# Optimization experiments

Measured on AMD Instinct MI355X. Metric: run time of the kernel, lower is better.

## Reference

```python
import jax, jax.numpy as jnp
import numpy as np

# CUBA-LIF constants (from LavaNetwork.__init__ with beta=0.95)
THRESHOLD = 1.0
CURRENT_DECAY = 1.0   # current[t] = (1-1.0)*current[t-1] + input[t] == input[t]
VOLTAGE_DECAY = 1.0 - 0.95  # = 0.05, so v[t] = 0.95*v[t-1] + cur[t]

N_INPUT, N_HIDDEN, N_OUTPUT = 512, 2048, 4 * 64
B, T = 32, 1024


def setup_inputs() -> dict:
    key = jax.random.key(0)
    kx, k1, k2, k3, k4 = jax.random.split(key, 5)
    x = (jax.random.uniform(kx, (B, N_INPUT, T)) < 0.1).astype(jnp.float32)
    # learned params (Linear with bias); small scale so spiking is reasonable
    w1 = jax.random.normal(k1, (N_HIDDEN, N_INPUT), dtype=jnp.float32) * (1.0 / np.sqrt(N_INPUT))
    b1 = jax.random.normal(k2, (N_HIDDEN,), dtype=jnp.float32) * 0.01
    w2 = jax.random.normal(k3, (N_OUTPUT, N_HIDDEN), dtype=jnp.float32) * (1.0 / np.sqrt(N_HIDDEN))
    b2 = jax.random.normal(k4, (N_OUTPUT,), dtype=jnp.float32) * 0.01
    return {"x": x, "w1": w1, "b1": b1, "w2": w2, "b2": b2}


def _cuba_lif(cur):
    """CUBA neuron with current_decay=1 (current==synaptic input),
    leaky-integrate voltage, fire at threshold, reset voltage to 0.
    cur: (B, N, T) -> spikes (B, N, T)."""
    beta_v = 1.0 - VOLTAGE_DECAY  # 0.95

    def step(v, c_t):
        v = v * beta_v + c_t
        s = (v >= THRESHOLD).astype(v.dtype)
        v = v * (1.0 - s)  # reset-to-zero on spike (Loihi behavior)
        return v, s

    cur_t = jnp.moveaxis(cur, -1, 0)  # (T, B, N)
    v0 = jnp.zeros(cur.shape[:-1], cur.dtype)
    _, spk = jax.lax.scan(step, v0, cur_t)
    return jnp.moveaxis(spk, 0, -1)  # (B, N, T)


def reference(x, w1, b1, w2, b2):
    # layer 1: synapse (einsum 'bit,oi->bot' + bias) -> CUBA neuron
    cur1 = jnp.einsum('bit,oi->bot', x, w1) + b1[None, :, None]
    spk1 = _cuba_lif(cur1)
    # layer 2
    cur2 = jnp.einsum('bit,oi->bot', spk1, w2) + b2[None, :, None]
    spk2 = _cuba_lif(cur2)
    return (spk1, spk2)
```

## Files before the change

kernel.cpp:

```cpp
#include <hip/hip_runtime.h>


typedef int i32x4 __attribute__((ext_vector_type(4)));
typedef _Float16 f16x8 __attribute__((ext_vector_type(8)));
typedef _Float16 f16x4 __attribute__((ext_vector_type(4)));
typedef float f32x4 __attribute__((ext_vector_type(4)));

#define GLDS(g, l) __builtin_amdgcn_global_load_lds( \
    (const __attribute__((address_space(1))) void*)(g), \
    (__attribute__((address_space(3))) void*)(l), 16, 0, 0)

#define INV231 4.656612873077392578125e-10


__global__ __launch_bounds__(256) void prep_w8(const float* __restrict__ A,
                                               signed char* __restrict__ wp,
                                               int M, int K)
{
    long gt = (long)blockIdx.x * 256 + threadIdx.x;
    int kq4 = K >> 2;
    int m = (int)(gt / kq4), kq = (int)(gt % kq4);
    int k0 = kq * 4;
    int kt = k0 >> 6, kin = k0 & 63;
    int cw = ((kin >> 4) ^ (m >> 1)) & 3;
    float4 w = *(const float4*)&A[(long)m * K + k0];
    float wv[4] = {w.x, w.y, w.z, w.w};
    int pack[4] = {0, 0, 0, 0};
#pragma unroll
    for (int e = 0; e < 4; e++) {
        long k64 = (long)rint((double)wv[e] * 2147483648.0);
#pragma unroll
        for (int j = 0; j < 3; j++) {
            long r = ((k64 + 128) & 255) - 128;
            pack[j] |= ((int)r & 255) << (e * 8);
            k64 = (k64 - r) >> 8;
        }
        pack[3] |= ((int)k64 & 255) << (e * 8);
    }
#pragma unroll
    for (int p = 0; p < 4; p++)
        *(int*)&wp[(((long)kt * 4 + p) * M + m) * 64 + cw * 16 + (kin & 15)] = pack[p];
}

__global__ __launch_bounds__(256) void prep_x8(const float* __restrict__ x,
                                               unsigned char* __restrict__ xt)
{
    __shared__ float xs[64][68];
    const int b = blockIdx.z, i0 = blockIdx.y * 64, t0 = blockIdx.x * 64;
    const float* xb = x + ((long)b * 512 + i0) * 1024 + t0;
#pragma unroll
    for (int p = 0; p < 4; p++) {
        int f = threadIdx.x + p * 256;
        int i = f >> 4, t4 = (f & 15) * 4;
        *(float4*)&xs[i][t4] = *(const float4*)&xb[(long)i * 1024 + t4];
    }
    __syncthreads();
    int tt = threadIdx.x >> 2, c = threadIdx.x & 3;
    unsigned char bytes[16];
#pragma unroll
    for (int j = 0; j < 16; j++)
        bytes[j] = (unsigned char)xs[c * 16 + j][tt];
    *(uint4*)&xt[(((long)b * 8 + (i0 >> 6)) * 1024 + t0 + tt) * 64 + c * 16] =
        *(uint4*)bytes;
}

__global__ __launch_bounds__(320, 1) void gemm_lif1(
    const signed char* __restrict__ wp,
    const unsigned char* __restrict__ act,
    const float* __restrict__ bias,
    unsigned char* __restrict__ spk8,
    float* __restrict__ spk1)
{
    __shared__ signed char Ws[8][4][64][64];
    __shared__ float cs[2][64][64];

    const int m0 = blockIdx.x * 64, b = blockIdx.y;
    const int tid = threadIdx.x, lane = tid & 63, wave = tid >> 6;
    const int lm = lane & 15, lq = lane >> 4;
    const int fro = ((lq ^ (lm >> 1)) & 3) * 16;
    const unsigned char* ab = act + (long)b * 8 * 1024 * 64;

    unsigned char* sp8 = spk8 + (((long)b * 32 + (m0 >> 6)) * 1024) * 64 + lane;
    float* sp1 = spk1 + ((long)b * 2048 + m0) * 1024;

    i32x4 areg[4][4];
    double bv = 0.0;

    if (wave < 4) {
        const int gl_row = lane >> 2, gl_col = (lane & 3) * 16;
#pragma unroll
        for (int j = 0; j < 8; ++j) {
            const int r = wave + 4 * j;
            const int kt = r >> 2, pl = r & 3;
            const signed char* g = wp + ((long)r * 2048 + m0 + gl_row) * 64 + gl_col;
#pragma unroll
            for (int q = 0; q < 4; ++q)
                GLDS(g + q * 16 * 64, &Ws[kt][pl][q * 16][0]);
        }
        bv = (double)bias[m0 + wave * 16 + lm];
#pragma unroll
        for (int f = 0; f < 4; f++)
            areg[0][f] = *(const i32x4*)
                &ab[((long)(f * 16 + lm)) * 64 + lq * 16];
#pragma unroll
        for (int f = 0; f < 4; f++)
            areg[1][f] = *(const i32x4*)
                &ab[((long)1 * 1024 + f * 16 + lm) * 64 + lq * 16];
    }
    __syncthreads();

    double u = 0.0;
    bool sprev = false;

    for (int p = 0; p < 17; ++p) {
        if (wave < 4 && p < 16) {
            i32x4 acc[4][4];
#pragma unroll
            for (int pp = 0; pp < 4; pp++)
#pragma unroll
                for (int f = 0; f < 4; f++) acc[pp][f] = (i32x4)0;

            i32x4 wreg[4];
            wreg[0] = *(const i32x4*)&Ws[0][0][wave * 16 + lm][fro];
            wreg[1] = *(const i32x4*)&Ws[0][1][wave * 16 + lm][fro];

#pragma unroll
            for (int kk = 0; kk < 8; ++kk) {
                {
                    int vn = p * 8 + kk + 2;
                    if (vn > 127) vn = 127;
                    const int pn = vn >> 3, kn = vn & 7;
                    const long tt = (long)pn * 64 + lm;
#pragma unroll
                    for (int f = 0; f < 4; f++)
                        areg[(kk + 2) & 3][f] = *(const i32x4*)
                            &ab[((long)kn * 1024 + tt + f * 16) * 64 + lq * 16];
                }
                __builtin_amdgcn_s_setprio(1);
#pragma unroll
                for (int pl = 0; pl < 4; pl++) {
                    const int q = kk * 4 + pl;
                    const int qn = q + 2;
                    if (qn < 32)
                        wreg[qn & 3] = *(const i32x4*)
                            &Ws[qn >> 2][qn & 3][wave * 16 + lm][fro];
#pragma unroll
                    for (int f = 0; f < 4; f++)
                        acc[pl][f] = __builtin_amdgcn_mfma_i32_16x16x64_i8(
                            areg[kk & 3][f], wreg[q & 3], acc[pl][f], 0, 0, 0);
                }
                __builtin_amdgcn_s_setprio(0);
            }
#pragma unroll
            for (int tf = 0; tf < 4; tf++)
#pragma unroll
                for (int r = 0; r < 4; r++) {
                    long T = acc[3][tf][r];
                    T = T * 256 + acc[2][tf][r];
                    T = T * 256 + acc[1][tf][r];
                    T = T * 256 + acc[0][tf][r];
                    cs[p & 1][tf * 16 + lq * 4 + r][wave * 16 + lm] =
                        (float)((double)T * INV231 + bv);
                }
        }
        if (wave == 4 && p >= 1) {
            const int pq = p - 1, buf = pq & 1;
            float cvA[32], cvB[32];
#pragma unroll
            for (int j = 0; j < 32; ++j) cvA[j] = cs[buf][j][lane];
#pragma unroll
            for (int j = 0; j < 32; ++j) cvB[j] = cs[buf][32 + j][lane];
            unsigned mwordA = 0, mwordB = 0;
#pragma unroll
            for (int j = 0; j < 32; ++j) {
                double c = (double)cvA[j];
                double a = 0.95 * u + c;
                u = sprev ? c : a;
                bool s = (u >= 1.0);
                mwordA |= (s ? 1u : 0u) << j;
                sprev = s;
                sp8[(long)(pq * 64 + j) * 64] = s ? 1 : 0;
            }
#pragma unroll
            for (int j = 0; j < 32; ++j) {
                double c = (double)cvB[j];
                double a = 0.95 * u + c;
                u = sprev ? c : a;
                bool s = (u >= 1.0);
                mwordB |= (s ? 1u : 0u) << j;
                sprev = s;
                sp8[(long)(pq * 64 + 32 + j) * 64] = s ? 1 : 0;
            }
            float* sp1t = sp1 + pq * 64 + lane;
#pragma unroll 4
            for (int mm = 0; mm < 64; ++mm) {
                unsigned wa = (unsigned)__shfl((int)mwordA, mm);
                unsigned wb = (unsigned)__shfl((int)mwordB, mm);
                unsigned sel = (lane < 32) ? wa : wb;
                sp1t[(long)mm * 1024] =
                    ((sel >> (lane & 31)) & 1u) ? 1.f : 0.f;
            }
        }
        asm volatile("s_waitcnt lgkmcnt(0)" ::: "memory");
        __builtin_amdgcn_s_barrier();
        __builtin_amdgcn_sched_barrier(0);
    }
}

template <bool TRANS, int NITER, int CHUNK>
__global__ __launch_bounds__(256, 2) void gemm_i8(
    const signed char* __restrict__ wp,
    const unsigned char* __restrict__ act,
    const float* __restrict__ bias,
    float* __restrict__ C,
    int M)
{
    constexpr int NCHUNK = NITER / CHUNK;
    __shared__ signed char Ws[CHUNK][4][32][64];

    const int b = blockIdx.y;
    const int m0 = blockIdx.z * 32, t0 = blockIdx.x * 256;
    const int tid = threadIdx.x, lane = tid & 63, wave = tid >> 6;
    const int wt = t0 + wave * 64;
    const int lm = lane & 15, lq = lane >> 4;
    const int fro = ((lq ^ (lm >> 1)) & 3) * 16;
    const int gl_row = lane >> 2, gl_col = (lane & 3) * 16;

    const unsigned char* ab = act + (long)b * NITER * 1024 * 64;

    auto stage = [&](int cc) {
#pragma unroll
        for (int j = 0; j < CHUNK; ++j) {
            const int r = wave + 4 * j;
            const int kt = r >> 2, p = r & 3;
            const long kg = ((long)(cc * CHUNK + kt) * 4 + p);
            const signed char* g = wp + (kg * M + m0 + gl_row) * 64 + gl_col;
            GLDS(g, &Ws[kt][p][0][0]);
            GLDS(g + 16 * 64, &Ws[kt][p][16][0]);
        }
    };

    i32x4 acc[4][8];
#pragma unroll
    for (int p = 0; p < 4; p++)
#pragma unroll
        for (int q = 0; q < 8; q++) acc[p][q] = (i32x4)0;

    stage(0);
    i32x4 areg[2][4];
#pragma unroll
    for (int f = 0; f < 4; f++)
        areg[0][f] = *(const i32x4*)&ab[((long)(wt + f * 16 + lm)) * 64 + lq * 16];
    __syncthreads();

    for (int c = 0; c < NCHUNK; ++c) {
#pragma unroll
        for (int kk = 0; kk < CHUNK; ++kk) {
            {
                const int itv = c * CHUNK + kk;
                const long nx = (itv + 1 < NITER) ? itv + 1 : itv;
#pragma unroll
                for (int f = 0; f < 4; f++)
                    areg[(kk + 1) & 1][f] = *(const i32x4*)
                        &ab[(nx * 1024 + wt + f * 16 + lm) * 64 + lq * 16];
            }
#pragma unroll
            for (int p = 0; p < 4; p++) {
                i32x4 w0 = *(const i32x4*)&Ws[kk][p][lm][fro];
                i32x4 w1 = *(const i32x4*)&Ws[kk][p][16 + lm][fro];
                if (TRANS) {
#pragma unroll
                    for (int f = 0; f < 4; f++) {
                        acc[p][f * 2 + 0] = __builtin_amdgcn_mfma_i32_16x16x64_i8(
                            areg[kk & 1][f], w0, acc[p][f * 2 + 0], 0, 0, 0);
                        acc[p][f * 2 + 1] = __builtin_amdgcn_mfma_i32_16x16x64_i8(
                            areg[kk & 1][f], w1, acc[p][f * 2 + 1], 0, 0, 0);
                    }
                } else {
#pragma unroll
                    for (int f = 0; f < 4; f++) {
                        acc[p][0 + f] = __builtin_amdgcn_mfma_i32_16x16x64_i8(
                            w0, areg[kk & 1][f], acc[p][0 + f], 0, 0, 0);
                        acc[p][4 + f] = __builtin_amdgcn_mfma_i32_16x16x64_i8(
                            w1, areg[kk & 1][f], acc[p][4 + f], 0, 0, 0);
                    }
                }
            }
        }
        if (c + 1 < NCHUNK) {
            __syncthreads();
            stage(c + 1);
            __syncthreads();
        }
    }

    if (TRANS) {
        double bv[2];
        bv[0] = (double)bias[m0 + lm];
        bv[1] = (double)bias[m0 + 16 + lm];
        float* Cb = C + (long)b * 1024 * M;
#pragma unroll
        for (int tf = 0; tf < 4; tf++)
#pragma unroll
            for (int r = 0; r < 4; r++) {
                const int trow = wt + tf * 16 + lq * 4 + r;
#pragma unroll
                for (int mf = 0; mf < 2; mf++) {
                    long T = acc[3][tf * 2 + mf][r];
                    T = T * 256 + acc[2][tf * 2 + mf][r];
                    T = T * 256 + acc[1][tf * 2 + mf][r];
                    T = T * 256 + acc[0][tf * 2 + mf][r];
                    Cb[(long)trow * M + m0 + mf * 16 + lm] =
                        (float)((double)T * INV231 + bv[mf]);
                }
            }
    } else {
        float* Cb = C + (long)b * M * 1024;
#pragma unroll
        for (int mf = 0; mf < 2; mf++)
#pragma unroll
            for (int r = 0; r < 4; r++) {
                const int mrow = m0 + mf * 16 + lq * 4 + r;
                const double bv = (double)bias[mrow];
#pragma unroll
                for (int tf = 0; tf < 4; tf++) {
                    long T = acc[3][mf * 4 + tf][r];
                    T = T * 256 + acc[2][mf * 4 + tf][r];
                    T = T * 256 + acc[1][mf * 4 + tf][r];
                    T = T * 256 + acc[0][mf * 4 + tf][r];
                    Cb[(long)mrow * 1024 + wt + tf * 16 + lm] =
                        (float)((double)T * INV231 + bv);
                }
            }
    }
}

template <int RPB>
__global__ __launch_bounds__(256) void lif_lds(float* __restrict__ cur)
{
    __shared__ float cs[RPB][36];
    const long rowbase = (long)blockIdx.x * RPB;
    float* base = cur + rowbase * 1024;
    const int tid = threadIdx.x;
    double v = 0.0;
    const int NV = RPB * 32 / 4;
    for (int tc = 0; tc < 1024; tc += 32) {
        for (int f = tid; f < NV; f += 256) {
            int row = f >> 3, t4 = (f & 7) * 4;
            *(float4*)&cs[row][t4] = *(const float4*)&base[(long)row * 1024 + tc + t4];
        }
        __syncthreads();
        if (tid < RPB) {
            float cv[32];
#pragma unroll
            for (int j = 0; j < 32; j++) cv[j] = cs[tid][j];
#pragma unroll
            for (int j = 0; j < 32; j++) {
                v = 0.95 * v + (double)cv[j];
                bool s = v >= 1.0;
                cs[tid][j] = s ? 1.f : 0.f;
                if (s) v = 0.0;
            }
        }
        __syncthreads();
        for (int f = tid; f < NV; f += 256) {
            int row = f >> 3, t4 = (f & 7) * 4;
            *(float4*)&base[(long)row * 1024 + tc + t4] = *(float4*)&cs[row][t4];
        }
        __syncthreads();
    }
}


__device__ inline void split3(float w, _Float16& q0, _Float16& q1, _Float16& q2) {
    float p0 = rintf(w * 4096.f) * 2.44140625e-4f;
    float r1 = w - p0;
    float p1s = rintf(r1 * 8388608.f) * 2.44140625e-4f;
    float r2 = r1 - p1s * 4.8828125e-4f;
    float p2s = rintf(r2 * 1.7179869184e10f) * 1.220703125e-4f;
    q0 = (_Float16)p0; q1 = (_Float16)p1s; q2 = (_Float16)p2s;
}

__global__ __launch_bounds__(256) void gemm_f16x3_kernel(
    const float* __restrict__ A, const float* __restrict__ Bmat,
    const float* __restrict__ bias, float* __restrict__ C,
    int M, int N, int K, long sB, long sC)
{
    __shared__ _Float16 As[3][128][40];
    __shared__ _Float16 Bsh[128][40];
    const int batch = blockIdx.z;
    const float* Bp = Bmat + (long)batch * sB;
    float* Cp = C + (long)batch * sC;
    const int m0 = blockIdx.y * 128, n0 = blockIdx.x * 128;
    const int tid = threadIdx.x, lane = tid & 63, wave = tid >> 6;
    const int wrow = (wave >> 1) * 64, wcol = (wave & 1) * 64;
    const int lm = lane & 15, lq = lane >> 4;
    const int a_mo = tid >> 3, a_kc = (tid & 7) * 4;
    const int b_kq = tid >> 5, b_nq = tid & 31;

    f32x4 acc[3][4][4];
#pragma unroll
    for (int p = 0; p < 3; p++)
#pragma unroll
        for (int i = 0; i < 4; i++)
#pragma unroll
            for (int j = 0; j < 4; j++) acc[p][i][j] = (f32x4)0.f;

    for (int k0 = 0; k0 < K; k0 += 32) {
#pragma unroll
        for (int i = 0; i < 4; i++) {
            const int m = i * 32 + a_mo;
            float4 w = *(const float4*)&A[(long)(m0 + m) * K + k0 + a_kc];
            _Float16 a0[4], a1[4], a2[4];
            split3(w.x, a0[0], a1[0], a2[0]);
            split3(w.y, a0[1], a1[1], a2[1]);
            split3(w.z, a0[2], a1[2], a2[2]);
            split3(w.w, a0[3], a1[3], a2[3]);
            *(f16x4*)&As[0][m][a_kc] = (f16x4){a0[0], a0[1], a0[2], a0[3]};
            *(f16x4*)&As[1][m][a_kc] = (f16x4){a1[0], a1[1], a1[2], a1[3]};
            *(f16x4*)&As[2][m][a_kc] = (f16x4){a2[0], a2[1], a2[2], a2[3]};
        }
        {
            float4 r0 = *(const float4*)&Bp[(long)(k0 + b_kq * 4 + 0) * N + n0 + b_nq * 4];
            float4 r1 = *(const float4*)&Bp[(long)(k0 + b_kq * 4 + 1) * N + n0 + b_nq * 4];
            float4 r2 = *(const float4*)&Bp[(long)(k0 + b_kq * 4 + 2) * N + n0 + b_nq * 4];
            float4 r3 = *(const float4*)&Bp[(long)(k0 + b_kq * 4 + 3) * N + n0 + b_nq * 4];
            *(f16x4*)&Bsh[b_nq * 4 + 0][b_kq * 4] =
                (f16x4){(_Float16)r0.x, (_Float16)r1.x, (_Float16)r2.x, (_Float16)r3.x};
            *(f16x4*)&Bsh[b_nq * 4 + 1][b_kq * 4] =
                (f16x4){(_Float16)r0.y, (_Float16)r1.y, (_Float16)r2.y, (_Float16)r3.y};
            *(f16x4*)&Bsh[b_nq * 4 + 2][b_kq * 4] =
                (f16x4){(_Float16)r0.z, (_Float16)r1.z, (_Float16)r2.z, (_Float16)r3.z};
            *(f16x4*)&Bsh[b_nq * 4 + 3][b_kq * 4] =
                (f16x4){(_Float16)r0.w, (_Float16)r1.w, (_Float16)r2.w, (_Float16)r3.w};
        }
        __syncthreads();
        f16x8 bf[4];
#pragma unroll
        for (int j = 0; j < 4; j++)
            bf[j] = *(const f16x8*)&Bsh[wcol + j * 16 + lm][lq * 8];
#pragma unroll
        for (int p = 0; p < 3; p++) {
            f16x8 af[4];
#pragma unroll
            for (int i = 0; i < 4; i++)
                af[i] = *(const f16x8*)&As[p][wrow + i * 16 + lm][lq * 8];
#pragma unroll
            for (int i = 0; i < 4; i++)
#pragma unroll
                for (int j = 0; j < 4; j++)
                    acc[p][i][j] = __builtin_amdgcn_mfma_f32_16x16x32_f16(
                        af[i], bf[j], acc[p][i][j], 0, 0, 0);
        }
        __syncthreads();
    }
#pragma unroll
    for (int i = 0; i < 4; i++)
#pragma unroll
        for (int r = 0; r < 4; r++) {
            const int row = m0 + wrow + i * 16 + lq * 4 + r;
            const double bv = (double)bias[row];
#pragma unroll
            for (int j = 0; j < 4; j++) {
                double s = (double)acc[0][i][j][r]
                         + (double)acc[1][i][j][r] * 4.8828125e-4
                         + (double)acc[2][i][j][r] * 4.76837158203125e-7 + bv;
                Cp[(long)row * N + n0 + wcol + j * 16 + lm] = (float)s;
            }
        }
}

__global__ __launch_bounds__(256) void lif_rows(float* __restrict__ data,
                                                long nrows, int T)
{
    long r = (long)blockIdx.x * blockDim.x + threadIdx.x;
    if (r >= nrows) return;
    float* p = data + r * (long)T;
    double v = 0.0;
    for (int t = 0; t < T; t += 4) {
        float4 c = *(float4*)(p + t);
        float4 s;
        v = 0.95 * v + (double)c.x; s.x = (v >= 1.0) ? 1.f : 0.f; if (v >= 1.0) v = 0.0;
        v = 0.95 * v + (double)c.y; s.y = (v >= 1.0) ? 1.f : 0.f; if (v >= 1.0) v = 0.0;
        v = 0.95 * v + (double)c.z; s.z = (v >= 1.0) ? 1.f : 0.f; if (v >= 1.0) v = 0.0;
        v = 0.95 * v + (double)c.w; s.w = (v >= 1.0) ? 1.f : 0.f; if (v >= 1.0) v = 0.0;
        *(float4*)(p + t) = s;
    }
}


extern "C" void kernel_launch(void* const* d_in, const int* in_sizes, int n_in,
                              void* d_out, int out_size, void* d_ws, size_t ws_size,
                              hipStream_t stream)
{
    const float* x  = (const float*)d_in[0];
    const float* w1 = (const float*)d_in[1];
    const float* b1 = (const float*)d_in[2];
    const float* w2 = (const float*)d_in[3];
    const float* b2 = (const float*)d_in[4];

    float* out  = (float*)d_out;
    float* spk1 = out;
    float* spk2 = out + (long)32 * 2048 * 1024;

    const size_t WP1 = 4194304;
    const size_t WP2 = 2097152;
    const size_t X8T = 16777216;
    const size_t SPK = 67108864;
    const size_t NEED = WP1 + WP2 + X8T + SPK;

    if (ws_size >= NEED) {
        char* ws = (char*)d_ws;
        signed char* wp1 = (signed char*)ws;
        signed char* wp2 = (signed char*)(ws + WP1);
        unsigned char* x8t = (unsigned char*)(ws + WP1 + WP2);
        unsigned char* spk8 = (unsigned char*)(ws + WP1 + WP2 + X8T);

        prep_w8<<<1024, 256, 0, stream>>>(w1, wp1, 2048, 512);
        prep_w8<<<512, 256, 0, stream>>>(w2, wp2, 256, 2048);
        prep_x8<<<dim3(16, 8, 32), 256, 0, stream>>>(x, x8t);

        gemm_lif1<<<dim3(32, 32), 320, 0, stream>>>(wp1, x8t, b1, spk8, spk1);

        gemm_i8<false, 32, 8><<<dim3(4, 32, 8), 256, 0, stream>>>(
            wp2, spk8, b2, spk2, 256);
        lif_lds<32><<<256, 256, 0, stream>>>(spk2);
    } else {
        gemm_f16x3_kernel<<<dim3(8, 16, 32), 256, 0, stream>>>(
            w1, x, b1, spk1, 2048, 1024, 512, (long)512 * 1024, (long)2048 * 1024);
        lif_rows<<<(65536 + 255) / 256, 256, 0, stream>>>(spk1, 65536, 1024);
        gemm_f16x3_kernel<<<dim3(8, 2, 32), 256, 0, stream>>>(
            w2, spk1, b2, spk2, 256, 1024, 2048, (long)2048 * 1024, (long)256 * 1024);
        lif_rows<<<(8192 + 255) / 256, 256, 0, stream>>>(spk2, 8192, 1024);
    }
}
```

Measured before the change: 749.3 us.

## Offload spike output stores from LIF wave to GEMM waves via mask buffer

```diff
diff --git a/kernel.cpp b/kernel.cpp
--- a/kernel.cpp
+++ b/kernel.cpp
@@ -68,6 +68,7 @@
     const signed char* __restrict__ wp,
     const unsigned char* __restrict__ act,
     const float* __restrict__ bias,
+    unsigned* __restrict__ mask_ws,
     unsigned char* __restrict__ spk8,
     float* __restrict__ spk1)
 {
@@ -80,9 +81,6 @@
     const int fro = ((lq ^ (lm >> 1)) & 3) * 16;
     const unsigned char* ab = act + (long)b * 8 * 1024 * 64;
 
-    unsigned char* sp8 = spk8 + (((long)b * 32 + (m0 >> 6)) * 1024) * 64 + lane;
-    float* sp1 = spk1 + ((long)b * 2048 + m0) * 1024;
-
     i32x4 areg[4][4];
     double bv = 0.0;
 
@@ -112,17 +110,13 @@
     double u = 0.0;
     bool sprev = false;
 
-    for (int p = 0; p < 17; ++p) {
+    for (int p = 0; p < 18; ++p) {
         if (wave < 4 && p < 16) {
             i32x4 acc[4][4];
 #pragma unroll
             for (int pp = 0; pp < 4; pp++)
 #pragma unroll
                 for (int f = 0; f < 4; f++) acc[pp][f] = (i32x4)0;
-
-            i32x4 wreg[4];
-            wreg[0] = *(const i32x4*)&Ws[0][0][wave * 16 + lm][fro];
-            wreg[1] = *(const i32x4*)&Ws[0][1][wave * 16 + lm][fro];
 
 #pragma unroll
             for (int kk = 0; kk < 8; ++kk) {
@@ -139,15 +133,11 @@
                 __builtin_amdgcn_s_setprio(1);
 #pragma unroll
                 for (int pl = 0; pl < 4; pl++) {
-                    const int q = kk * 4 + pl;
-                    const int qn = q + 2;
-                    if (qn < 32)
-                        wreg[qn & 3] = *(const i32x4*)
-                            &Ws[qn >> 2][qn & 3][wave * 16 + lm][fro];
+                    i32x4 w0 = *(const i32x4*)&Ws[kk][pl][wave * 16 + lm][fro];
 #pragma unroll
                     for (int f = 0; f < 4; f++)
                         acc[pl][f] = __builtin_amdgcn_mfma_i32_16x16x64_i8(
-                            areg[kk & 3][f], wreg[q & 3], acc[pl][f], 0, 0, 0);
+                            areg[kk & 3][f], w0, acc[pl][f], 0, 0, 0);
                 }
                 __builtin_amdgcn_s_setprio(0);
             }
@@ -163,7 +153,31 @@
                         (float)((double)T * INV231 + bv);
                 }
         }
-        if (wave == 4 && p >= 1) {
+        if (wave < 4 && p >= 2) {
+            const int pq2 = p - 2;
+            const unsigned myA =
+                mask_ws[((long)b * 32 + pq2 * 2 + 0) * 2048 + m0 + lane];
+            const unsigned myB =
+                mask_ws[((long)b * 32 + pq2 * 2 + 1) * 2048 + m0 + lane];
+            unsigned char* s8 =
+                spk8 + (((long)b * 32 + (m0 >> 6)) * 1024 + pq2 * 64) * 64 + lane;
+#pragma unroll
+            for (int jj = 0; jj < 16; ++jj) {
+                const int t = wave * 16 + jj;
+                const unsigned word = (t < 32) ? myA : myB;
+                s8[(long)t * 64] = (unsigned char)((word >> (t & 31)) & 1u);
+            }
+            float* s1 = spk1 + ((long)b * 2048 + m0 + wave * 16) * 1024
+                        + pq2 * 64 + lane;
+#pragma unroll
+            for (int rr = 0; rr < 16; ++rr) {
+                const unsigned wA = (unsigned)__shfl((int)myA, wave * 16 + rr);
+                const unsigned wB = (unsigned)__shfl((int)myB, wave * 16 + rr);
+                const unsigned sel = (lane < 32) ? wA : wB;
+                s1[(long)rr * 1024] = ((sel >> (lane & 31)) & 1u) ? 1.f : 0.f;
+            }
+        }
+        if (wave == 4 && p >= 1 && p <= 16) {
             const int pq = p - 1, buf = pq & 1;
             float cvA[32], cvB[32];
 #pragma unroll
@@ -179,7 +193,6 @@
                 bool s = (u >= 1.0);
                 mwordA |= (s ? 1u : 0u) << j;
                 sprev = s;
-                sp8[(long)(pq * 64 + j) * 64] = s ? 1 : 0;
             }
 #pragma unroll
             for (int j = 0; j < 32; ++j) {
@@ -189,17 +202,10 @@
                 bool s = (u >= 1.0);
                 mwordB |= (s ? 1u : 0u) << j;
                 sprev = s;
-                sp8[(long)(pq * 64 + 32 + j) * 64] = s ? 1 : 0;
-            }
-            float* sp1t = sp1 + pq * 64 + lane;
-#pragma unroll 4
-            for (int mm = 0; mm < 64; ++mm) {
-                unsigned wa = (unsigned)__shfl((int)mwordA, mm);
-                unsigned wb = (unsigned)__shfl((int)mwordB, mm);
-                unsigned sel = (lane < 32) ? wa : wb;
-                sp1t[(long)mm * 1024] =
-                    ((sel >> (lane & 31)) & 1u) ? 1.f : 0.f;
-            }
+            }
+            mask_ws[((long)b * 32 + pq * 2 + 0) * 2048 + m0 + lane] = mwordA;
+            mask_ws[((long)b * 32 + pq * 2 + 1) * 2048 + m0 + lane] = mwordB;
+            asm volatile("s_waitcnt vmcnt(0)" ::: "memory");
         }
         asm volatile("s_waitcnt lgkmcnt(0)" ::: "memory");
         __builtin_amdgcn_s_barrier();
@@ -507,7 +513,8 @@
     const size_t WP2 = 2097152;
     const size_t X8T = 16777216;
     const size_t SPK = 67108864;
-    const size_t NEED = WP1 + WP2 + X8T + SPK;
+    const size_t MSK = 8388608;
+    const size_t NEED = WP1 + WP2 + X8T + SPK + MSK;
 
     if (ws_size >= NEED) {
         char* ws = (char*)d_ws;
@@ -515,12 +522,14 @@
         signed char* wp2 = (signed char*)(ws + WP1);
         unsigned char* x8t = (unsigned char*)(ws + WP1 + WP2);
         unsigned char* spk8 = (unsigned char*)(ws + WP1 + WP2 + X8T);
+        unsigned* mask_ws = (unsigned*)(ws + WP1 + WP2 + X8T + SPK);
 
         prep_w8<<<1024, 256, 0, stream>>>(w1, wp1, 2048, 512);
         prep_w8<<<512, 256, 0, stream>>>(w2, wp2, 256, 2048);
         prep_x8<<<dim3(16, 8, 32), 256, 0, stream>>>(x, x8t);
 
-        gemm_lif1<<<dim3(32, 32), 320, 0, stream>>>(wp1, x8t, b1, spk8, spk1);
+        gemm_lif1<<<dim3(32, 32), 320, 0, stream>>>(
+            wp1, x8t, b1, mask_ws, spk8, spk1);
 
         gemm_i8<false, 32, 8><<<dim3(4, 32, 8), 256, 0, stream>>>(
             wp2, spk8, b2, spk2, 256);
```

Result: faster. 672.5 us (-10.3%).
